# Optimization experiments

Hardware: AMD Instinct MI355X
Metric: run time of the kernel (lower is better)

The kernel has to match this reference:

```python
import jax, jax.numpy as jnp
import numpy as np

N_NODES = 50000
IN_DIM = 128
HID = 128
N_EDGES = 600000
BN_EPS = 1e-5


def setup_inputs() -> dict:
    key = jax.random.key(0)
    ks = jax.random.split(key, 8)
    x = jax.random.normal(ks[0], (N_NODES, IN_DIM), dtype=jnp.float32)
    edge_index = jax.random.randint(ks[1], (2, N_EDGES), 0, N_NODES, dtype=jnp.int64)
    s1 = 1.0 / np.sqrt(IN_DIM)
    s2 = 1.0 / np.sqrt(HID)
    W1 = jax.random.uniform(ks[2], (HID, IN_DIM), jnp.float32, -s1, s1)
    b1 = jax.random.uniform(ks[3], (HID,), jnp.float32, -s1, s1)
    gamma = jnp.ones((HID,), jnp.float32)
    beta = jnp.zeros((HID,), jnp.float32)
    W2 = jax.random.uniform(ks[4], (HID, HID), jnp.float32, -s2, s2)
    b2 = jax.random.uniform(ks[5], (HID,), jnp.float32, -s2, s2)
    Wres = jax.random.uniform(ks[6], (HID, IN_DIM), jnp.float32, -s1, s1)
    return {"x": x, "edge_index": edge_index, "W1": W1, "b1": b1,
            "gamma": gamma, "beta": beta, "W2": W2, "b2": b2, "Wres": Wres}


def reference(x, edge_index, W1, b1, gamma, beta, W2, b2, Wres):
    # GINConv aggregation (eps=0): h_v = x_v + sum_{u in N(v)} x_u
    src, dst = edge_index[0], edge_index[1]
    agg = jax.ops.segment_sum(x[src], dst, num_segments=N_NODES)  # [N, in_dim]
    h = x + agg
    # MLP: Linear -> BatchNorm (batch stats, training mode) -> LeakyReLU(0.01) -> Linear
    h = h @ W1.T + b1  # [N, hid]
    mu = jnp.mean(h, axis=0)
    var = jnp.mean(jnp.square(h - mu), axis=0)  # biased var, as torch BN training
    h = (h - mu) * jax.lax.rsqrt(var + BN_EPS) * gamma + beta
    h = jax.nn.leaky_relu(h, negative_slope=0.01)
    h = h @ W2.T + b2
    # residual projection + final leaky relu
    x_res = x @ Wres.T
    return jax.nn.leaky_relu(h + x_res, negative_slope=0.2)
```

## Files before the change

kernel.cpp:

```cpp
#include <hip/hip_runtime.h>

#define N_NODES 50000
#define N_EDGES 600000
#define BN_EPS 1e-5f
#define NBKT 782
#define BKT_CAP 1024
#define CHUNK 4096
#define CS_BLOCKS 147

typedef __bf16 bf16x8 __attribute__((ext_vector_type(8)));
typedef float f32x4 __attribute__((ext_vector_type(4)));

__device__ __forceinline__ float leaky(float v, float slope) {
    return v > 0.f ? v : v * slope;
}

__device__ __forceinline__ bf16x8 pack8(float4 v0, float4 v1) {
    bf16x8 b;
    b[0] = (__bf16)v0.x; b[1] = (__bf16)v0.y; b[2] = (__bf16)v0.z; b[3] = (__bf16)v0.w;
    b[4] = (__bf16)v1.x; b[5] = (__bf16)v1.y; b[6] = (__bf16)v1.z; b[7] = (__bf16)v1.w;
    return b;
}

__global__ __launch_bounds__(256) void k_fused(
        const int* __restrict__ ei, int* __restrict__ cnt, unsigned* __restrict__ coarse,
        const float4* __restrict__ x4, uint4* __restrict__ xb4,
        const float* __restrict__ W1, const float* __restrict__ W2,
        const float* __restrict__ Wres, uint4* __restrict__ w1f, uint4* __restrict__ w2f) {
    int tid = threadIdx.x;
    if (blockIdx.x == CS_BLOCKS + 3125) {
        #pragma unroll
        for (int i = 0; i < 8; ++i) {
            int fid = tid + i * 256;
            int lane = fid & 63, ks = (fid >> 6) & 3, jt = fid >> 8;
            const float* wp = W1 + (jt * 16 + (lane & 15)) * 128 + ks * 32 + ((lane >> 4) << 3);
            w1f[fid] = __builtin_bit_cast(uint4, pack8(*(const float4*)wp, *(const float4*)(wp + 4)));
        }
        #pragma unroll
        for (int i = 0; i < 16; ++i) {
            int fid = tid + i * 256;
            int lane = fid & 63, ks = (fid >> 6) & 7, jt = fid >> 9;
            const float* wp = (ks < 4 ? W2 : Wres) + (jt * 16 + (lane & 15)) * 128
                              + (ks & 3) * 32 + ((lane >> 4) << 3);
            w2f[fid] = __builtin_bit_cast(uint4, pack8(*(const float4*)wp, *(const float4*)(wp + 4)));
        }
        return;
    }
    if (blockIdx.x >= CS_BLOCKS) {
        int g = (blockIdx.x - CS_BLOCKS) * 256 + tid;
        float4 v0 = x4[g * 2], v1 = x4[g * 2 + 1];
        xb4[g] = __builtin_bit_cast(uint4, pack8(v0, v1));
        return;
    }
    __shared__ unsigned lcnt[NBKT];
    __shared__ unsigned lbase[NBKT];
    for (int i = tid; i < NBKT; i += 256) lcnt[i] = 0;
    __syncthreads();
    int e0 = blockIdx.x * CHUNK;
    unsigned pk[16], meta[16];
    #pragma unroll
    for (int i = 0; i < 16; ++i) {
        int e = e0 + tid + i * 256;
        if (e < N_EDGES) {
            int s = ei[e];
            int d = ei[N_EDGES + e];
            int b = d >> 6;
            pk[i] = (unsigned)s | ((unsigned)(d & 63) << 16);
            unsigned r = atomicAdd(&lcnt[b], 1u);
            meta[i] = (unsigned)b | (r << 16);
        }
    }
    __syncthreads();
    for (int b = tid; b < NBKT; b += 256) {
        unsigned c = lcnt[b];
        lbase[b] = c ? (unsigned)atomicAdd(&cnt[b], (int)c) : 0u;
    }
    __syncthreads();
    #pragma unroll
    for (int i = 0; i < 16; ++i) {
        int e = e0 + tid + i * 256;
        if (e < N_EDGES) {
            unsigned b = meta[i] & 0xFFFFu;
            unsigned p = lbase[b] + (meta[i] >> 16);
            if (p < BKT_CAP) coarse[b * BKT_CAP + p] = pk[i];
        }
    }
}

__global__ __launch_bounds__(512) void k_agg(
        const int* __restrict__ cnt, const unsigned* __restrict__ coarse,
        const uint4* __restrict__ xb4, uint4* __restrict__ h4) {
    __shared__ unsigned hist[64];
    __shared__ unsigned offs[64];
    __shared__ unsigned short ssrc[BKT_CAP];
    int tid = threadIdx.x;
    int b = blockIdx.x;
    int m = cnt[b];
    if (m > BKT_CAP) m = BKT_CAP;

    if (tid < 64) hist[tid] = 0;
    __syncthreads();

    unsigned pk[2], rk[2];
    #pragma unroll
    for (int i = 0; i < 2; ++i) {
        int idx = tid + i * 512;
        if (idx < m) {
            pk[i] = coarse[b * BKT_CAP + idx];
            rk[i] = atomicAdd(&hist[pk[i] >> 16], 1u);
        }
    }
    __syncthreads();
    if (tid < 64) {
        unsigned v = hist[tid];
        unsigned inc = v;
        #pragma unroll
        for (int d = 1; d < 64; d <<= 1) {
            unsigned t = __shfl_up(inc, d);
            if (tid >= d) inc += t;
        }
        offs[tid] = inc - v;
    }
    __syncthreads();
    #pragma unroll
    for (int i = 0; i < 2; ++i) {
        int idx = tid + i * 512;
        if (idx < m) ssrc[offs[pk[i] >> 16] + rk[i]] = (unsigned short)(pk[i] & 0xFFFFu);
    }
    __syncthreads();

    int li = tid & 15, grp = tid >> 4;
    #pragma unroll
    for (int it = 0; it < 2; ++it) {
        int dl = grp + it * 32;
        int v = b * 64 + dl;
        if (v >= N_NODES) continue;
        bf16x8 self = __builtin_bit_cast(bf16x8, xb4[v * 16 + li]);
        float acc[8];
        #pragma unroll
        for (int e = 0; e < 8; ++e) acc[e] = (float)self[e];
        unsigned e0 = offs[dl], e1 = e0 + hist[dl];
        for (unsigned e = e0; e < e1; ++e) {
            int s = ssrc[e];
            bf16x8 u = __builtin_bit_cast(bf16x8, xb4[s * 16 + li]);
            #pragma unroll
            for (int k = 0; k < 8; ++k) acc[k] += (float)u[k];
        }
        bf16x8 o;
        #pragma unroll
        for (int k = 0; k < 8; ++k) o[k] = (__bf16)acc[k];
        h4[v * 16 + li] = __builtin_bit_cast(uint4, o);
    }
}

__global__ __launch_bounds__(256) void k_gemm1(
        const uint4* __restrict__ hb4, const uint4* __restrict__ w1f,
        const float* __restrict__ b1, __bf16* __restrict__ h1b,
        float* __restrict__ stats) {
    __shared__ float sred[4][128];
    __shared__ float s2red[4][128];
    int tid = threadIdx.x;
    int wv = tid >> 6, lane = tid & 63;
    int strip = blockIdx.x * 4 + wv;
    bool valid = strip < 3125;
    int node0 = (valid ? strip : 3124) * 16;

    bf16x8 a[4];
    int rbase = (node0 + (lane & 15)) * 16 + (lane >> 4);
    #pragma unroll
    for (int ks = 0; ks < 4; ++ks)
        a[ks] = __builtin_bit_cast(bf16x8, hb4[rbase + ks * 4]);

    #pragma unroll
    for (int jt = 0; jt < 8; ++jt) {
        f32x4 acc = {0.f, 0.f, 0.f, 0.f};
        #pragma unroll
        for (int ks = 0; ks < 4; ++ks) {
            bf16x8 b = __builtin_bit_cast(bf16x8, w1f[(jt * 4 + ks) * 64 + lane]);
            acc = __builtin_amdgcn_mfma_f32_16x16x32_bf16(a[ks], b, acc, 0, 0, 0);
        }
        int j = jt * 16 + (lane & 15);
        float bias = b1[j];
        int nb = node0 + ((lane >> 4) << 2);
        float s = 0.f, s2 = 0.f;
        if (valid) {
            #pragma unroll
            for (int r = 0; r < 4; ++r) {
                float v = acc[r] + bias;
                h1b[(nb + r) * 128 + j] = (__bf16)v;
                s += v; s2 += v * v;
            }
        }
        s  += __shfl_down(s, 32);  s  += __shfl_down(s, 16);
        s2 += __shfl_down(s2, 32); s2 += __shfl_down(s2, 16);
        if (lane < 16) { sred[wv][j] = s; s2red[wv][j] = s2; }
    }
    __syncthreads();
    if (tid < 128) {
        atomicAdd(&stats[tid],       sred[0][tid] + sred[1][tid] + sred[2][tid] + sred[3][tid]);
        atomicAdd(&stats[128 + tid], s2red[0][tid] + s2red[1][tid] + s2red[2][tid] + s2red[3][tid]);
    }
}

__global__ __launch_bounds__(256) void k_gemm2(
        const uint4* __restrict__ h1b4, const uint4* __restrict__ xb4,
        const uint4* __restrict__ w2f, const float* __restrict__ b2,
        const float* __restrict__ stats, const float* __restrict__ gamma,
        const float* __restrict__ beta, float* __restrict__ out) {
    __shared__ float bl[128], scl[128], shl[128];
    int tid = threadIdx.x;
    if (tid < 128) {
        float inv = 1.f / (float)N_NODES;
        float mu = stats[tid] * inv;
        float var = stats[128 + tid] * inv - mu * mu;
        float rs = rsqrtf(var + BN_EPS);
        float sc = gamma[tid] * rs;
        bl[tid]  = b2[tid];
        scl[tid] = sc;
        shl[tid] = beta[tid] - mu * sc;
    }
    __syncthreads();

    int wv = tid >> 6, lane = tid & 63;
    int strip = blockIdx.x * 4 + wv;
    if (strip >= 3125) return;
    int node0 = strip * 16;
    int rbase = (node0 + (lane & 15)) * 16 + (lane >> 4);
    int kbase = (lane >> 4) << 3;

    bf16x8 a[8];
    #pragma unroll
    for (int ks = 0; ks < 4; ++ks) {
        bf16x8 hv = __builtin_bit_cast(bf16x8, h1b4[rbase + ks * 4]);
        #pragma unroll
        for (int e = 0; e < 8; ++e) {
            int k = kbase + ks * 32 + e;
            float t = (float)hv[e] * scl[k] + shl[k];
            a[ks][e] = (__bf16)leaky(t, 0.01f);
        }
    }
    #pragma unroll
    for (int ks = 0; ks < 4; ++ks)
        a[4 + ks] = __builtin_bit_cast(bf16x8, xb4[rbase + ks * 4]);

    #pragma unroll
    for (int jt = 0; jt < 8; ++jt) {
        f32x4 acc = {0.f, 0.f, 0.f, 0.f};
        #pragma unroll
        for (int ks = 0; ks < 8; ++ks) {
            bf16x8 b = __builtin_bit_cast(bf16x8, w2f[(jt * 8 + ks) * 64 + lane]);
            acc = __builtin_amdgcn_mfma_f32_16x16x32_bf16(a[ks], b, acc, 0, 0, 0);
        }
        int j = jt * 16 + (lane & 15);
        float bias = bl[j];
        int nb = node0 + ((lane >> 4) << 2);
        #pragma unroll
        for (int r = 0; r < 4; ++r) {
            float v = acc[r] + bias;
            out[(nb + r) * 128 + j] = leaky(v, 0.2f);
        }
    }
}

extern "C" void kernel_launch(void* const* d_in, const int* in_sizes, int n_in,
                              void* d_out, int out_size, void* d_ws, size_t ws_size,
                              hipStream_t stream) {
    const float* x     = (const float*)d_in[0];
    const int*   ei    = (const int*)d_in[1];
    const float* W1    = (const float*)d_in[2];
    const float* b1    = (const float*)d_in[3];
    const float* gamma = (const float*)d_in[4];
    const float* beta  = (const float*)d_in[5];
    const float* W2    = (const float*)d_in[6];
    const float* b2    = (const float*)d_in[7];
    const float* Wres  = (const float*)d_in[8];
    float* out = (float*)d_out;

    char* ws = (char*)d_ws;
    uint4*    xb4    = (uint4*)ws;
    uint4*    h4     = (uint4*)(ws + 12800000);
    __bf16*   h1b    = (__bf16*)(ws + 25600000);
    unsigned* coarse = (unsigned*)(ws + 38400000);
    int*      cnt    = (int*)(ws + 41700000);
    float*    stats  = (float*)(ws + 41700000 + NBKT * 4);
    uint4*    w1f    = (uint4*)(ws + 42000000);
    uint4*    w2f    = w1f + 2048;

    hipMemsetAsync(cnt, 0, (NBKT + 512) * 4, stream);
    k_fused<<<CS_BLOCKS + 3125 + 1, 256, 0, stream>>>(ei, cnt, coarse, (const float4*)x, xb4,
                                                      W1, W2, Wres, w1f, w2f);
    k_agg<<<NBKT, 512, 0, stream>>>(cnt, coarse, xb4, h4);
    k_gemm1<<<782, 256, 0, stream>>>(h4, w1f, b1, h1b, stats);
    k_gemm2<<<782, 256, 0, stream>>>((const uint4*)h1b, xb4, w2f, b2, stats, gamma, beta, out);
}
```

Before: 108.4 us.

## Fuse neighbor aggregation with first GEMM via swizzled LDS tile

Merges the aggregation kernel and the first linear layer into one kernel. Aggregated bf16 rows for the block's 64 nodes are kept in a XOR-swizzled shared-memory tile and fed straight to MFMA, so the intermediate h buffer no longer makes a global write and read round trip and one launch is dropped. Each block now runs 8 waves covering 4 row groups times 2 column halves. The gather loop is also unrolled by four so more loads are in flight per lane. The cost is extra LDS per block, which may reduce occupancy.

```diff
diff --git a/kernel.cpp b/kernel.cpp
--- a/kernel.cpp
+++ b/kernel.cpp
@@ -87,12 +87,17 @@
     }
 }
 
-__global__ __launch_bounds__(512) void k_agg(
+__global__ __launch_bounds__(512) void k_agg1(
         const int* __restrict__ cnt, const unsigned* __restrict__ coarse,
-        const uint4* __restrict__ xb4, uint4* __restrict__ h4) {
+        const uint4* __restrict__ xb4, const uint4* __restrict__ w1f,
+        const float* __restrict__ b1, __bf16* __restrict__ h1b,
+        float* __restrict__ stats) {
     __shared__ unsigned hist[64];
     __shared__ unsigned offs[64];
     __shared__ unsigned short ssrc[BKT_CAP];
+    __shared__ uint4 hls[1024];
+    __shared__ float sred[8][64];
+    __shared__ float s2red[8][64];
     int tid = threadIdx.x;
     int b = blockIdx.x;
     int m = cnt[b];
@@ -100,7 +105,6 @@
 
     if (tid < 64) hist[tid] = 0;
     __syncthreads();
-
     unsigned pk[2], rk[2];
     #pragma unroll
     for (int i = 0; i < 2; ++i) {
@@ -129,59 +133,68 @@
     }
     __syncthreads();
 
-    int li = tid & 15, grp = tid >> 4;
-    #pragma unroll
-    for (int it = 0; it < 2; ++it) {
-        int dl = grp + it * 32;
-        int v = b * 64 + dl;
-        if (v >= N_NODES) continue;
-        bf16x8 self = __builtin_bit_cast(bf16x8, xb4[v * 16 + li]);
-        float acc[8];
-        #pragma unroll
-        for (int e = 0; e < 8; ++e) acc[e] = (float)self[e];
-        unsigned e0 = offs[dl], e1 = e0 + hist[dl];
-        for (unsigned e = e0; e < e1; ++e) {
-            int s = ssrc[e];
-            bf16x8 u = __builtin_bit_cast(bf16x8, xb4[s * 16 + li]);
-            #pragma unroll
-            for (int k = 0; k < 8; ++k) acc[k] += (float)u[k];
-        }
-        bf16x8 o;
-        #pragma unroll
-        for (int k = 0; k < 8; ++k) o[k] = (__bf16)acc[k];
-        h4[v * 16 + li] = __builtin_bit_cast(uint4, o);
-    }
-}
-
-__global__ __launch_bounds__(256) void k_gemm1(
-        const uint4* __restrict__ hb4, const uint4* __restrict__ w1f,
-        const float* __restrict__ b1, __bf16* __restrict__ h1b,
-        float* __restrict__ stats) {
-    __shared__ float sred[4][128];
-    __shared__ float s2red[4][128];
-    int tid = threadIdx.x;
+    {
+        int li = tid & 15, grp = tid >> 4;
+        #pragma unroll
+        for (int it = 0; it < 2; ++it) {
+            int dl = grp + it * 32;
+            int v = b * 64 + dl;
+            if (v < N_NODES) {
+                bf16x8 self = __builtin_bit_cast(bf16x8, xb4[v * 16 + li]);
+                float acc[8];
+                #pragma unroll
+                for (int k = 0; k < 8; ++k) acc[k] = (float)self[k];
+                unsigned e0 = offs[dl], e1 = e0 + hist[dl];
+                unsigned e = e0;
+                for (; e + 4 <= e1; e += 4) {
+                    int s0 = ssrc[e], s1 = ssrc[e + 1], s2 = ssrc[e + 2], s3 = ssrc[e + 3];
+                    bf16x8 u0 = __builtin_bit_cast(bf16x8, xb4[s0 * 16 + li]);
+                    bf16x8 u1 = __builtin_bit_cast(bf16x8, xb4[s1 * 16 + li]);
+                    bf16x8 u2 = __builtin_bit_cast(bf16x8, xb4[s2 * 16 + li]);
+                    bf16x8 u3 = __builtin_bit_cast(bf16x8, xb4[s3 * 16 + li]);
+                    #pragma unroll
+                    for (int k = 0; k < 8; ++k)
+                        acc[k] += ((float)u0[k] + (float)u1[k]) + ((float)u2[k] + (float)u3[k]);
+                }
+                for (; e < e1; ++e) {
+                    int s = ssrc[e];
+                    bf16x8 u = __builtin_bit_cast(bf16x8, xb4[s * 16 + li]);
+                    #pragma unroll
+                    for (int k = 0; k < 8; ++k) acc[k] += (float)u[k];
+                }
+                bf16x8 o;
+                #pragma unroll
+                for (int k = 0; k < 8; ++k) o[k] = (__bf16)acc[k];
+                hls[dl * 16 + (li ^ (dl & 7))] = __builtin_bit_cast(uint4, o);
+            }
+        }
+    }
+    __syncthreads();
+
     int wv = tid >> 6, lane = tid & 63;
-    int strip = blockIdx.x * 4 + wv;
-    bool valid = strip < 3125;
-    int node0 = (valid ? strip : 3124) * 16;
+    int rgrp = wv & 3, jh = wv >> 2;
+    int node0 = b * 64 + rgrp * 16;
+    bool valid = node0 < N_NODES;
+    int dl0 = rgrp * 16 + (lane & 15);
+    int q = lane >> 4;
 
     bf16x8 a[4];
-    int rbase = (node0 + (lane & 15)) * 16 + (lane >> 4);
     #pragma unroll
     for (int ks = 0; ks < 4; ++ks)
-        a[ks] = __builtin_bit_cast(bf16x8, hb4[rbase + ks * 4]);
-
-    #pragma unroll
-    for (int jt = 0; jt < 8; ++jt) {
+        a[ks] = __builtin_bit_cast(bf16x8, hls[dl0 * 16 + ((ks * 4 + q) ^ (dl0 & 7))]);
+
+    #pragma unroll
+    for (int jt4 = 0; jt4 < 4; ++jt4) {
+        int jt = jh * 4 + jt4;
         f32x4 acc = {0.f, 0.f, 0.f, 0.f};
         #pragma unroll
         for (int ks = 0; ks < 4; ++ks) {
-            bf16x8 b = __builtin_bit_cast(bf16x8, w1f[(jt * 4 + ks) * 64 + lane]);
-            acc = __builtin_amdgcn_mfma_f32_16x16x32_bf16(a[ks], b, acc, 0, 0, 0);
+            bf16x8 bb = __builtin_bit_cast(bf16x8, w1f[(jt * 4 + ks) * 64 + lane]);
+            acc = __builtin_amdgcn_mfma_f32_16x16x32_bf16(a[ks], bb, acc, 0, 0, 0);
         }
         int j = jt * 16 + (lane & 15);
         float bias = b1[j];
-        int nb = node0 + ((lane >> 4) << 2);
+        int nb = node0 + (q << 2);
         float s = 0.f, s2 = 0.f;
         if (valid) {
             #pragma unroll
@@ -193,12 +206,18 @@
         }
         s  += __shfl_down(s, 32);  s  += __shfl_down(s, 16);
         s2 += __shfl_down(s2, 32); s2 += __shfl_down(s2, 16);
-        if (lane < 16) { sred[wv][j] = s; s2red[wv][j] = s2; }
+        if (lane < 16) {
+            sred[wv][jt4 * 16 + (lane & 15)] = s;
+            s2red[wv][jt4 * 16 + (lane & 15)] = s2;
+        }
     }
     __syncthreads();
     if (tid < 128) {
-        atomicAdd(&stats[tid],       sred[0][tid] + sred[1][tid] + sred[2][tid] + sred[3][tid]);
-        atomicAdd(&stats[128 + tid], s2red[0][tid] + s2red[1][tid] + s2red[2][tid] + s2red[3][tid]);
+        int half = tid >> 6, jj = tid & 63, w0 = half * 4;
+        atomicAdd(&stats[tid],
+                  sred[w0][jj] + sred[w0 + 1][jj] + sred[w0 + 2][jj] + sred[w0 + 3][jj]);
+        atomicAdd(&stats[128 + tid],
+                  s2red[w0][jj] + s2red[w0 + 1][jj] + s2red[w0 + 2][jj] + s2red[w0 + 3][jj]);
     }
 }
 
@@ -278,7 +297,6 @@
 
     char* ws = (char*)d_ws;
     uint4*    xb4    = (uint4*)ws;
-    uint4*    h4     = (uint4*)(ws + 12800000);
     __bf16*   h1b    = (__bf16*)(ws + 25600000);
     unsigned* coarse = (unsigned*)(ws + 38400000);
     int*      cnt    = (int*)(ws + 41700000);
@@ -289,7 +307,6 @@
     hipMemsetAsync(cnt, 0, (NBKT + 512) * 4, stream);
     k_fused<<<CS_BLOCKS + 3125 + 1, 256, 0, stream>>>(ei, cnt, coarse, (const float4*)x, xb4,
                                                       W1, W2, Wres, w1f, w2f);
-    k_agg<<<NBKT, 512, 0, stream>>>(cnt, coarse, xb4, h4);
-    k_gemm1<<<782, 256, 0, stream>>>(h4, w1f, b1, h1b, stats);
+    k_agg1<<<NBKT, 512, 0, stream>>>(cnt, coarse, xb4, w1f, b1, h1b, stats);
     k_gemm2<<<782, 256, 0, stream>>>((const uint4*)h1b, xb4, w2f, b2, stats, gamma, beta, out);
 }
```

Measured after the change: 97.84 us. 1.11x faster.
